# Performance work log

Measured on AMD Instinct MI355X. Metric: run time of the kernel, lower is better.

The kernel has to match this reference:

```python
import jax, jax.numpy as jnp
import numpy as np

D_MODEL = 2048
NUM_HEADS = 32
NUM_KV_HEADS = 8
D_K = D_MODEL // NUM_HEADS  # 64
GROUPS = NUM_HEADS // NUM_KV_HEADS  # 4
KV_DIM = NUM_KV_HEADS * D_K  # 512


def setup_inputs() -> dict:
    key = jax.random.key(0)
    ks = jax.random.split(key, 9)
    s = 0.02
    return {
        "x": jax.random.normal(ks[0], (2, 2048, D_MODEL), dtype=jnp.float32),
        "Wq": jax.random.normal(ks[1], (D_MODEL, D_MODEL), dtype=jnp.float32) * s,
        "bq": jnp.zeros((D_MODEL,), dtype=jnp.float32),
        "Wk": jax.random.normal(ks[2], (D_MODEL, KV_DIM), dtype=jnp.float32) * s,
        "bk": jnp.zeros((KV_DIM,), dtype=jnp.float32),
        "Wv": jax.random.normal(ks[3], (D_MODEL, KV_DIM), dtype=jnp.float32) * s,
        "bv": jnp.zeros((KV_DIM,), dtype=jnp.float32),
        "Wo": jax.random.normal(ks[4], (D_MODEL, D_MODEL), dtype=jnp.float32) * s,
        "bo": jnp.zeros((D_MODEL,), dtype=jnp.float32),
    }


def reference(x, Wq, bq, Wk, bk, Wv, bv, Wo, bo):
    B, S, _ = x.shape
    # projections
    Q = (x @ Wq + bq).reshape(B, S, NUM_HEADS, D_K).transpose(0, 2, 1, 3)      # [B,H,S,dk]
    K = (x @ Wk + bk).reshape(B, S, NUM_KV_HEADS, D_K).transpose(0, 2, 1, 3)   # [B,Hkv,S,dk]
    V = (x @ Wv + bv).reshape(B, S, NUM_KV_HEADS, D_K).transpose(0, 2, 1, 3)
    # repeat_interleave KV heads to match query heads
    K = jnp.repeat(K, GROUPS, axis=1)  # [B,H,S,dk]
    V = jnp.repeat(V, GROUPS, axis=1)
    scale = 1.0 / jnp.sqrt(jnp.asarray(D_K, dtype=x.dtype))
    scores = jnp.einsum("bhqd,bhkd->bhqk", Q, K) * scale  # [B,H,S,S]
    attn = jax.nn.softmax(scores, axis=-1)
    out = jnp.einsum("bhqk,bhkd->bhqd", attn, V)           # [B,H,S,dk]
    out = out.transpose(0, 2, 1, 3).reshape(B, S, D_MODEL)
    return out @ Wo + bo
```

## Files before the change

### kernel.cpp

```cpp
#include <hip/hip_runtime.h>
#include <hip/hip_bf16.h>
#include <stdint.h>

typedef __bf16 bf16;
typedef __bf16 bf16x8 __attribute__((ext_vector_type(8)));
typedef float  f32x2  __attribute__((ext_vector_type(2)));
typedef float  f32x4  __attribute__((ext_vector_type(4)));
typedef float  f32x16 __attribute__((ext_vector_type(16)));

#define D_MODEL 2048
#define KV_DIM  512
#define SEQ     2048
#define BATCH   2
#define MTOT    (BATCH*SEQ)
#define QKV_N   3072
#define QSCALE  (0.125f*1.44269504088896f)

#if __has_builtin(__builtin_amdgcn_exp2f)
#define EXP2(x) __builtin_amdgcn_exp2f(x)
#else
#define EXP2(x) exp2f(x)
#endif

__global__ __launch_bounds__(256) void cvt_f32_bf16(const float* __restrict__ in,
                                                    bf16* __restrict__ out, int n) {
  int i = (blockIdx.x * 256 + threadIdx.x) * 4;
  if (i < n) {
    float4 v = *reinterpret_cast<const float4*>(in + i);
    bf16 o[4] = {(bf16)v.x, (bf16)v.y, (bf16)v.z, (bf16)v.w};
    *reinterpret_cast<uint64_t*>(out + i) = *reinterpret_cast<const uint64_t*>(o);
  }
}

__global__ __launch_bounds__(256) void transpose_all(
    const float* __restrict__ Wq, const float* __restrict__ Wk,
    const float* __restrict__ Wv, const float* __restrict__ Wo,
    bf16* __restrict__ Wall, bf16* __restrict__ Wot) {
  const int z = blockIdx.z;
  const float* W; bf16* dst; int N;
  if (z == 0)      { W = Wq; dst = Wall;                          N = 2048; }
  else if (z == 1) { W = Wk; dst = Wall + (size_t)2048 * 2048;    N = 512;  }
  else if (z == 2) { W = Wv; dst = Wall + (size_t)2560 * 2048;    N = 512;  }
  else             { W = Wo; dst = Wot;                           N = 2048; }
  const int n0 = blockIdx.x * 64, k0 = blockIdx.y * 64;
  if (n0 >= N) return;
  __shared__ float tile[64][65];
  const int tx = threadIdx.x & 63;
  const int ty = threadIdx.x >> 6;
  #pragma unroll
  for (int i = ty; i < 64; i += 4)
    tile[i][tx] = W[(size_t)(k0 + i) * N + n0 + tx];
  __syncthreads();
  #pragma unroll
  for (int i = ty; i < 64; i += 4)
    dst[(size_t)(n0 + i) * 2048 + k0 + tx] = (bf16)tile[tx][i];
}

__global__ __launch_bounds__(256) void transpose_v(const bf16* __restrict__ QKV,
                                                   bf16* __restrict__ Vtg) {
  __shared__ bf16 t[64][72];
  const int st = blockIdx.x;
  const int bk = blockIdx.y;
  const int b = bk >> 3, kvh = bk & 7;
  const int tid = threadIdx.x;
  const int r = tid >> 2, c = (tid & 3) * 16;
  const bf16* src = QKV + (size_t)(b * SEQ + st * 64 + r) * QKV_N + 2560 + kvh * 64 + c;
  *(bf16x8*)&t[r][c]     = *(const bf16x8*)src;
  *(bf16x8*)&t[r][c + 8] = *(const bf16x8*)(src + 8);
  __syncthreads();
  bf16 tmp[16];
  #pragma unroll
  for (int j = 0; j < 16; ++j) tmp[j] = t[c + j][r];
  bf16* dst = Vtg + (size_t)(bk * 64 + r) * SEQ + st * 64 + c;
  *(bf16x8*)dst       = *(const bf16x8*)tmp;
  *(bf16x8*)(dst + 8) = *(const bf16x8*)(tmp + 8);
}

__device__ __forceinline__ void gload_lds16(const bf16* g, bf16* l) {
  __builtin_amdgcn_global_load_lds(
      (const __attribute__((address_space(1))) uint32_t*)g,
      (__attribute__((address_space(3))) uint32_t*)l, 16, 0, 0);
}

__device__ __forceinline__ uint32_t pk2(float a, float b) {
  union { bf16 h[2]; uint32_t u; } v;
  v.h[0] = (bf16)a; v.h[1] = (bf16)b;
  return v.u;
}

template<int NF, int OUT_BF16>
__global__ __launch_bounds__(512, 2) void gemm256(
    const bf16* __restrict__ A, const bf16* __restrict__ Bt,
    const float* __restrict__ b0, const float* __restrict__ b1,
    const float* __restrict__ b2, int sp1, int sp2, int nscale, float scale,
    void* __restrict__ Cout, int N, int K)
{
  __shared__ bf16 As[2][256 * 64];
  __shared__ bf16 Bs[2][NF * 64 * 64];

  const int tid = threadIdx.x, lane = tid & 63;
  const int wid = tid >> 6;
  const int wr = wid >> 1, wc = wid & 1;
  const int l31 = lane & 31, hi2 = lane >> 5;
  const int rx = l31 & 7;

  const int bid = blockIdx.y * 16 + blockIdx.x;
  const int swz = (bid & 7) * 32 + (bid >> 3);
  const int m0 = (swz >> 4) * 256, n0 = (swz & 15) * (NF * 64);

  const int srow = tid >> 3;
  const int schk = (tid & 7) ^ (srow & 7);
  const bf16* aSrc = A  + (size_t)(m0 + srow) * K + schk * 8;
  const bf16* bSrc = Bt + (size_t)(n0 + srow) * K + schk * 8;
  const size_t rstep = (size_t)64 * K;

  f32x16 acc[2][NF] = {};

  const int NT = K / 64;

#define G256_STAGE(T, BUF)                                            \
  {                                                                   \
    const bf16* a_ = aSrc + (T) * 64;                                 \
    _Pragma("unroll")                                                 \
    for (int j = 0; j < 4; ++j)                                       \
      gload_lds16(a_ + j * rstep, &As[BUF][j * 4096 + tid * 8]);      \
    const bf16* b_ = bSrc + (T) * 64;                                 \
    _Pragma("unroll")                                                 \
    for (int j = 0; j < NF; ++j)                                      \
      gload_lds16(b_ + j * rstep, &Bs[BUF][j * 4096 + tid * 8]);      \
  }

#define G256_WAITL()                                                  \
  if constexpr (NF == 3) asm volatile("s_waitcnt vmcnt(7)" ::: "memory"); \
  else                   asm volatile("s_waitcnt vmcnt(6)" ::: "memory");

#define G256_BODY(BUF)                                                \
  {                                                                   \
    _Pragma("unroll")                                                 \
    for (int ks = 0; ks < 4; ++ks) {                                  \
      bf16x8 af[2], bfv[NF];                                          \
      _Pragma("unroll")                                               \
      for (int m = 0; m < 2; ++m)                                     \
        af[m] = *(const bf16x8*)&As[BUF][(wr * 64 + m * 32 + l31) * 64 \
                                         + (((ks * 2 + hi2) ^ rx) * 8)]; \
      _Pragma("unroll")                                               \
      for (int n = 0; n < NF; ++n)                                    \
        bfv[n] = *(const bf16x8*)&Bs[BUF][(wc * (NF * 32) + n * 32 + l31) * 64 \
                                          + (((ks * 2 + hi2) ^ rx) * 8)]; \
      __builtin_amdgcn_s_setprio(1);                                  \
      _Pragma("unroll")                                               \
      for (int m = 0; m < 2; ++m)                                     \
        _Pragma("unroll")                                             \
        for (int n = 0; n < NF; ++n)                                  \
          acc[m][n] = __builtin_amdgcn_mfma_f32_32x32x16_bf16(        \
              af[m], bfv[n], acc[m][n], 0, 0, 0);                     \
      __builtin_amdgcn_s_setprio(0);                                  \
    }                                                                 \
  }

  G256_STAGE(0, 0)
  G256_STAGE(1, 1)
  G256_WAITL()
  __builtin_amdgcn_sched_barrier(0);
  __builtin_amdgcn_s_barrier();
  __builtin_amdgcn_sched_barrier(0);

  for (int t = 0; t < NT; t += 2) {
    #pragma unroll
    for (int u = 0; u < 2; ++u) {
      G256_BODY(u)
      __builtin_amdgcn_sched_barrier(0);
      __builtin_amdgcn_s_barrier();
      __builtin_amdgcn_sched_barrier(0);
      const int tt = t + u;
      if (tt < NT - 2) {
        G256_STAGE(tt + 2, u)
        G256_WAITL()
      } else {
        asm volatile("s_waitcnt vmcnt(0)" ::: "memory");
      }
      __builtin_amdgcn_sched_barrier(0);
      __builtin_amdgcn_s_barrier();
      __builtin_amdgcn_sched_barrier(0);
    }
  }

#undef G256_STAGE
#undef G256_WAITL
#undef G256_BODY

  const int cb = n0 + wc * (NF * 32) + l31;
  #pragma unroll
  for (int n = 0; n < NF; ++n) {
    const int col = cb + n * 32;
    float bv;
    if (col < sp1)      bv = b0[col];
    else if (col < sp2) bv = b1[col - sp1];
    else                bv = b2[col - sp2];
    const float scl = (col < nscale) ? scale : 1.0f;
    #pragma unroll
    for (int m = 0; m < 2; ++m) {
      const int rb = m0 + wr * 64 + m * 32 + 4 * hi2;
      #pragma unroll
      for (int r = 0; r < 16; ++r) {
        const int row = rb + (r & 3) + 8 * (r >> 2);
        const float v = (acc[m][n][r] + bv) * scl;
        if (OUT_BF16) ((bf16*)Cout)[(size_t)row * N + col] = (bf16)v;
        else          ((float*)Cout)[(size_t)row * N + col] = v;
      }
    }
  }
}

__global__ __launch_bounds__(256, 2) void attn_kernel(
    const bf16* __restrict__ QKV, const bf16* __restrict__ Vtg, bf16* __restrict__ ctx)
{
  __shared__ bf16 smem[4][64 * 64];

  const int tid = threadIdx.x, lane = tid & 63, wid = tid >> 6;
  const int l31 = lane & 31, hi = lane >> 5;
  const int qt = blockIdx.x & 7;
  const int bh = blockIdx.x >> 3;
  const int h = bh & 31, b = bh >> 5, kvh = h >> 2;

  const bf16* gK = QKV + (size_t)b * SEQ * QKV_N + 2048 + kvh * 64;
  const bf16* gV = Vtg + (size_t)(b * 8 + kvh) * 64 * SEQ;

  const int sr  = lane >> 3;
  const int scn = (lane & 7) ^ sr;

  bf16x8 qf[4], qf2[4];
  {
    const bf16* qp = QKV + (size_t)(b * SEQ + qt * 256 + wid * 64 + l31) * QKV_N + h * 64 + hi * 8;
    #pragma unroll
    for (int kt = 0; kt < 4; ++kt) qf[kt]  = *(const bf16x8*)(qp + kt * 16);
    const bf16* qp2 = qp + (size_t)32 * QKV_N;
    #pragma unroll
    for (int kt = 0; kt < 4; ++kt) qf2[kt] = *(const bf16x8*)(qp2 + kt * 16);
  }

  bf16x8 onesv;
  #pragma unroll
  for (int j = 0; j < 8; ++j) onesv[j] = (bf16)1.0f;

  f32x16 o0 = {}, o1 = {}, o2 = {}, o3 = {};
  f32x16 lacc = {}, lacc2 = {};

  const int row0 = (wid * 2 + 0) * 8 + sr;
  const int row1 = (wid * 2 + 1) * 8 + sr;
  const bf16* pK0 = gK + (size_t)row0 * QKV_N + scn * 8;
  const bf16* pK1 = gK + (size_t)row1 * QKV_N + scn * 8;
  const bf16* pV0 = gV + (size_t)row0 * SEQ + scn * 8;
  const bf16* pV1 = gV + (size_t)row1 * SEQ + scn * 8;

  gload_lds16(pK0, &smem[0][(wid * 2 + 0) * 512]);
  gload_lds16(pK1, &smem[0][(wid * 2 + 1) * 512]);
  gload_lds16(pV0, &smem[2][(wid * 2 + 0) * 512]);
  gload_lds16(pV1, &smem[2][(wid * 2 + 1) * 512]);
  pK0 += (size_t)64 * QKV_N; pK1 += (size_t)64 * QKV_N; pV0 += 64; pV1 += 64;
  __syncthreads();

  const int rx = l31 & 7;

#define PV_SET(SA, SB, OA, OB, LC)                                        \
    _Pragma("unroll")                                                     \
    for (int s = 0; s < 4; ++s) {                                         \
      const f32x16& sv = (s < 2) ? SA : SB;                               \
      const int rb = (s & 1) * 8;                                         \
      uint32_t Aw = pk2(sv[rb + 0], sv[rb + 1]);                          \
      uint32_t Bw = pk2(sv[rb + 2], sv[rb + 3]);                          \
      uint32_t Cw = pk2(sv[rb + 4], sv[rb + 5]);                          \
      uint32_t Dw = pk2(sv[rb + 6], sv[rb + 7]);                          \
      union { uint32_t w[4]; bf16x8 v; } pf;                              \
      auto rA = __builtin_amdgcn_permlane32_swap(Aw, Cw, false, false);   \
      auto rB = __builtin_amdgcn_permlane32_swap(Bw, Dw, false, false);   \
      pf.w[0] = rA[0]; pf.w[1] = rB[0]; pf.w[2] = rA[1]; pf.w[3] = rB[1]; \
      __builtin_amdgcn_s_setprio(1);                                      \
      OA = __builtin_amdgcn_mfma_f32_32x32x16_bf16(vf[s],     pf.v, OA, 0, 0, 0); \
      OB = __builtin_amdgcn_mfma_f32_32x32x16_bf16(vf[s + 4], pf.v, OB, 0, 0, 0); \
      LC = __builtin_amdgcn_mfma_f32_32x32x16_bf16(onesv,     pf.v, LC, 0, 0, 0); \
      __builtin_amdgcn_s_setprio(0);                                      \
    }

  for (int it = 0; it < 32; ++it) {
    const int cur = it & 1;
    if (it < 31) {
      gload_lds16(pK0, &smem[cur ^ 1][(wid * 2 + 0) * 512]);
      gload_lds16(pK1, &smem[cur ^ 1][(wid * 2 + 1) * 512]);
      gload_lds16(pV0, &smem[2 + (cur ^ 1)][(wid * 2 + 0) * 512]);
      gload_lds16(pV1, &smem[2 + (cur ^ 1)][(wid * 2 + 1) * 512]);
      pK0 += (size_t)64 * QKV_N; pK1 += (size_t)64 * QKV_N; pV0 += 64; pV1 += 64;
    }
    const bf16* Kb = smem[cur];
    const bf16* Vb = smem[2 + cur];

    bf16x8 kf[8];
    #pragma unroll
    for (int kt = 0; kt < 4; ++kt) {
      const int ck = hi + 2 * kt;
      kf[kt]     = *(const bf16x8*)(Kb + (size_t)l31 * 64        + ((ck ^ rx) * 8));
      kf[kt + 4] = *(const bf16x8*)(Kb + (size_t)(32 + l31) * 64 + ((ck ^ rx) * 8));
    }
    f32x16 s0v = {}, s1v = {}, s2v = {}, s3v = {};
    __builtin_amdgcn_s_setprio(1);
    #pragma unroll
    for (int kt = 0; kt < 4; ++kt) {
      s0v = __builtin_amdgcn_mfma_f32_32x32x16_bf16(kf[kt],     qf[kt],  s0v, 0, 0, 0);
      s1v = __builtin_amdgcn_mfma_f32_32x32x16_bf16(kf[kt + 4], qf[kt],  s1v, 0, 0, 0);
      s2v = __builtin_amdgcn_mfma_f32_32x32x16_bf16(kf[kt],     qf2[kt], s2v, 0, 0, 0);
      s3v = __builtin_amdgcn_mfma_f32_32x32x16_bf16(kf[kt + 4], qf2[kt], s3v, 0, 0, 0);
    }
    __builtin_amdgcn_s_setprio(0);

    bf16x8 vf[8];
    #pragma unroll
    for (int s = 0; s < 4; ++s) {
      const int ck = hi + 2 * s;
      vf[s]     = *(const bf16x8*)(Vb + (size_t)l31 * 64        + ((ck ^ rx) * 8));
      vf[s + 4] = *(const bf16x8*)(Vb + (size_t)(32 + l31) * 64 + ((ck ^ rx) * 8));
    }

    #pragma unroll
    for (int r = 0; r < 16; ++r) {
      s0v[r] = EXP2(s0v[r]); s1v[r] = EXP2(s1v[r]);
      s2v[r] = EXP2(s2v[r]); s3v[r] = EXP2(s3v[r]);
    }

    PV_SET(s0v, s1v, o0, o1, lacc)
    PV_SET(s2v, s3v, o2, o3, lacc2)
    __syncthreads();
  }
#undef PV_SET

#define WRITE_SET(OA, OB, LC, QOFF)                                        \
  {                                                                        \
    const float inv = 1.0f / LC[0];                                        \
    OA *= inv; OB *= inv;                                                  \
    uint32_t* ot = (uint32_t*)((bf16*)smem + wid * 2304);                  \
    _Pragma("unroll")                                                      \
    for (int r = 0; r < 16; r += 2) {                                      \
      const int d = (r & 3) + 8 * (r >> 2) + 4 * hi;                       \
      ot[l31 * 36 + (d >> 1)]        = pk2(OA[r], OA[r + 1]);              \
      ot[l31 * 36 + ((32 + d) >> 1)] = pk2(OB[r], OB[r + 1]);              \
    }                                                                      \
    __syncthreads();                                                       \
    {                                                                      \
      const int q2 = lane >> 1, hf = lane & 1;                             \
      const bf16* src = (const bf16*)smem + wid * 2304 + q2 * 72 + hf * 32;\
      bf16* dst = ctx + (size_t)(b * SEQ + qt * 256 + wid * 64 + (QOFF) + q2) * D_MODEL \
                      + h * 64 + hf * 32;                                  \
      _Pragma("unroll")                                                    \
      for (int k = 0; k < 4; ++k)                                          \
        *(bf16x8*)(dst + k * 8) = *(const bf16x8*)(src + k * 8);           \
    }                                                                      \
    __syncthreads();                                                       \
  }

  WRITE_SET(o0, o1, lacc, 0)
  WRITE_SET(o2, o3, lacc2, 32)
#undef WRITE_SET
}

extern "C" void kernel_launch(void* const* d_in, const int* in_sizes, int n_in,
                              void* d_out, int out_size, void* d_ws, size_t ws_size,
                              hipStream_t stream) {
  const float* x  = (const float*)d_in[0];
  const float* Wq = (const float*)d_in[1];
  const float* bq = (const float*)d_in[2];
  const float* Wk = (const float*)d_in[3];
  const float* bk = (const float*)d_in[4];
  const float* Wv = (const float*)d_in[5];
  const float* bv = (const float*)d_in[6];
  const float* Wo = (const float*)d_in[7];
  const float* bo = (const float*)d_in[8];
  float* out = (float*)d_out;

  char* ws = (char*)d_ws;
  size_t off = 0;
  bf16* xb   = (bf16*)(ws + off); off += (size_t)MTOT * D_MODEL * 2;
  bf16* Wall = (bf16*)(ws + off); off += (size_t)QKV_N * D_MODEL * 2;
  bf16* Wot  = (bf16*)(ws + off); off += (size_t)D_MODEL * D_MODEL * 2;
  bf16* QKV  = (bf16*)(ws + off); off += (size_t)MTOT * QKV_N * 2;
  bf16* ctx  = (bf16*)(ws + off); off += (size_t)MTOT * D_MODEL * 2;
  bf16* Vtg  = (bf16*)(ws + off); off += (size_t)16 * 64 * SEQ * 2;

  {
    int n = MTOT * D_MODEL;
    cvt_f32_bf16<<<n / 4 / 256, 256, 0, stream>>>(x, xb, n);
  }
  transpose_all<<<dim3(32, 32, 4), 256, 0, stream>>>(Wq, Wk, Wv, Wo, Wall, Wot);

  gemm256<3, 1><<<dim3(16, 16), 512, 0, stream>>>(
      xb, Wall, bq, bk, bv, 2048, 2560, 2048, QSCALE, QKV, QKV_N, D_MODEL);

  transpose_v<<<dim3(SEQ / 64, 16), 256, 0, stream>>>(QKV, Vtg);

  attn_kernel<<<dim3((SEQ / 256) * BATCH * 32), 256, 0, stream>>>(QKV, Vtg, ctx);

  gemm256<2, 0><<<dim3(16, 16), 512, 0, stream>>>(
      ctx, Wot, bo, bo, bo, 2048, 2048, 0, 1.0f, out, D_MODEL, D_MODEL);
}
```

Before: 219.1 us.

## Restructure GEMM main loop into interleaved 8-wave ping-pong schedule

Replaces the two-ahead prefetch GEMM loop with a one-ahead double-buffered schedule. Each K tile is split into four sub-steps that alternate LDS fragment reads, global-to-LDS loads for the next tile and MFMA bursts, with barriers between them. The goal is to spread global load issue across the compute phases and keep waves in lockstep so MFMA and memory overlap better. In exchange there are many more barriers and only one tile of prefetch depth, so memory latency may be exposed.

After: 216.3 us. About the same (-1.3%).

```diff
diff --git a/kernel.cpp b/kernel.cpp
--- a/kernel.cpp
+++ b/kernel.cpp
@@ -118,35 +118,18 @@
 
   const int NT = K / 64;
 
-#define G256_STAGE(T, BUF)                                            \
-  {                                                                   \
-    const bf16* a_ = aSrc + (T) * 64;                                 \
-    _Pragma("unroll")                                                 \
-    for (int j = 0; j < 4; ++j)                                       \
-      gload_lds16(a_ + j * rstep, &As[BUF][j * 4096 + tid * 8]);      \
-    const bf16* b_ = bSrc + (T) * 64;                                 \
-    _Pragma("unroll")                                                 \
-    for (int j = 0; j < NF; ++j)                                      \
-      gload_lds16(b_ + j * rstep, &Bs[BUF][j * 4096 + tid * 8]);      \
-  }
-
-#define G256_WAITL()                                                  \
-  if constexpr (NF == 3) asm volatile("s_waitcnt vmcnt(7)" ::: "memory"); \
-  else                   asm volatile("s_waitcnt vmcnt(6)" ::: "memory");
-
-#define G256_BODY(BUF)                                                \
-  {                                                                   \
-    _Pragma("unroll")                                                 \
-    for (int ks = 0; ks < 4; ++ks) {                                  \
+#define G8_READ(BUF, KS)                                              \
       bf16x8 af[2], bfv[NF];                                          \
       _Pragma("unroll")                                               \
       for (int m = 0; m < 2; ++m)                                     \
         af[m] = *(const bf16x8*)&As[BUF][(wr * 64 + m * 32 + l31) * 64 \
-                                         + (((ks * 2 + hi2) ^ rx) * 8)]; \
+                                         + ((((KS) * 2 + hi2) ^ rx) * 8)]; \
       _Pragma("unroll")                                               \
       for (int n = 0; n < NF; ++n)                                    \
         bfv[n] = *(const bf16x8*)&Bs[BUF][(wc * (NF * 32) + n * 32 + l31) * 64 \
-                                          + (((ks * 2 + hi2) ^ rx) * 8)]; \
+                                          + ((((KS) * 2 + hi2) ^ rx) * 8)];
+
+#define G8_MMA()                                                      \
       __builtin_amdgcn_s_setprio(1);                                  \
       _Pragma("unroll")                                               \
       for (int m = 0; m < 2; ++m)                                     \
@@ -154,40 +137,70 @@
         for (int n = 0; n < NF; ++n)                                  \
           acc[m][n] = __builtin_amdgcn_mfma_f32_32x32x16_bf16(        \
               af[m], bfv[n], acc[m][n], 0, 0, 0);                     \
-      __builtin_amdgcn_s_setprio(0);                                  \
+      __builtin_amdgcn_s_setprio(0);
+
+#define G8_TILE(U, TT)                                                \
+  {                                                                   \
+    const int tt = (TT);                                              \
+    const bool more = (tt < NT - 1);                                  \
+    const bf16* a_ = aSrc + (size_t)(tt + 1) * 64;                    \
+    const bf16* b_ = bSrc + (size_t)(tt + 1) * 64;                    \
+    {                               \
+      G8_READ(U, 0)                                                   \
+      if (more) {                                                     \
+        _Pragma("unroll")                                             \
+        for (int j = 0; j < 4; ++j)                                   \
+          gload_lds16(a_ + j * rstep, &As[(U) ^ 1][j * 4096 + tid * 8]); \
+      }                                                               \
+      __builtin_amdgcn_s_barrier();                                   \
+      G8_MMA()                                                        \
+      __builtin_amdgcn_s_barrier();                                   \
     }                                                                 \
-  }
-
-  G256_STAGE(0, 0)
-  G256_STAGE(1, 1)
-  G256_WAITL()
-  __builtin_amdgcn_sched_barrier(0);
-  __builtin_amdgcn_s_barrier();
-  __builtin_amdgcn_sched_barrier(0);
+    {                               \
+      G8_READ(U, 1)                                                   \
+      if (more) {                                                     \
+        _Pragma("unroll")                                             \
+        for (int j = 0; j < NF; ++j)                                  \
+          gload_lds16(b_ + j * rstep, &Bs[(U) ^ 1][j * 4096 + tid * 8]); \
+      }                                                               \
+      __builtin_amdgcn_s_barrier();                                   \
+      G8_MMA()                                                        \
+      __builtin_amdgcn_s_barrier();                                   \
+    }                                                                 \
+    {                                                  \
+      G8_READ(U, 2)                                                   \
+      __builtin_amdgcn_s_barrier();                                   \
+      G8_MMA()                                                        \
+      __builtin_amdgcn_s_barrier();                                   \
+    }                                                                 \
+    { \
+      G8_READ(U, 3)                                                   \
+      __builtin_amdgcn_s_barrier();                                   \
+      G8_MMA()                                                        \
+      asm volatile("s_waitcnt vmcnt(0)" ::: "memory");                \
+      __builtin_amdgcn_s_barrier();                                   \
+    }                                                                 \
+  }
+
+  {
+    #pragma unroll
+    for (int j = 0; j < 4; ++j)
+      gload_lds16(aSrc + j * rstep, &As[0][j * 4096 + tid * 8]);
+    #pragma unroll
+    for (int j = 0; j < NF; ++j)
+      gload_lds16(bSrc + j * rstep, &Bs[0][j * 4096 + tid * 8]);
+    asm volatile("s_waitcnt vmcnt(0)" ::: "memory");
+    __builtin_amdgcn_s_barrier();
+  }
 
   for (int t = 0; t < NT; t += 2) {
-    #pragma unroll
-    for (int u = 0; u < 2; ++u) {
-      G256_BODY(u)
-      __builtin_amdgcn_sched_barrier(0);
-      __builtin_amdgcn_s_barrier();
-      __builtin_amdgcn_sched_barrier(0);
-      const int tt = t + u;
-      if (tt < NT - 2) {
-        G256_STAGE(tt + 2, u)
-        G256_WAITL()
-      } else {
-        asm volatile("s_waitcnt vmcnt(0)" ::: "memory");
-      }
-      __builtin_amdgcn_sched_barrier(0);
-      __builtin_amdgcn_s_barrier();
-      __builtin_amdgcn_sched_barrier(0);
-    }
-  }
-
-#undef G256_STAGE
-#undef G256_WAITL
-#undef G256_BODY
+    G8_TILE(0, t)
+    G8_TILE(1, t + 1)
+  }
+
+#undef G8_READ
+#undef G8_MMA
+#undef G8_TILE
 
   const int cb = n0 + wc * (NF * 32) + l31;
   #pragma unroll
```
